# Kernel optimization log

Measured on AMD Instinct MI355X. Metric: run time of the kernel, lower is better.

## Reference

```python
import jax, jax.numpy as jnp
import numpy as np


def setup_inputs() -> dict:
    key = jax.random.key(0)
    k1, k2, k3 = jax.random.split(key, 3)
    T, B, C, H, W = 8, 4, 128, 96, 96
    h = w = 384  # original visibility-map resolution
    values = jax.random.normal(k1, (T + 1, B, C, H, W), jnp.float32)
    tvmap = jax.random.uniform(k2, (B, 1, h, w), jnp.float32)
    rvmaps = jax.random.uniform(k3, (T, B, 1, h, w), jnp.float32)
    return {"values": values, "tvmap": tvmap, "rvmaps": rvmaps}


def _resize_bin(m, H, W):
    # bilinear resize (half-pixel centers == torch align_corners=False), then > 0.5 threshold
    r = jax.image.resize(m, m.shape[:-2] + (H, W), method="bilinear")
    return (r > 0.5).astype(m.dtype)


def reference(values, tvmap, rvmaps):
    t_feat = values[0]          # [B,C,H,W]
    r_feats = values[1:]        # [T,B,C,H,W]
    T, B, C, H, W = r_feats.shape

    tv = _resize_bin(tvmap, H, W)                           # [B,1,H,W]
    rv = jax.vmap(lambda m: _resize_bin(m, H, W))(rvmaps)   # [T,B,1,H,W]
    vmap_ = tv[None] * rv                                   # [T,B,1,H,W]

    # per-frame masked similarity score gs
    gs = jnp.sum(vmap_ * t_feat[None] * r_feats, axis=(-1, -2, -3))  # [T,B]
    v_sum = jnp.sum(vmap_[:, :, 0], axis=(-1, -2))                   # [T,B]
    empty = v_sum < 1e-4
    gs = jnp.where(empty, 0.0, gs) / (v_sum + empty.astype(gs.dtype)) / C

    gss = gs.transpose(1, 0)[:, None, :, None, None]   # [B,1,T,1,1]
    vmaps = rv.transpose(1, 2, 0, 3, 4)                # [B,1,T,H,W]

    # masked softmax over frame axis (dim=2) with zero-guard
    mv = gss * vmaps
    mx = jnp.max(mv, axis=2, keepdims=True)
    me = jnp.exp(mv - mx) * vmaps
    ms = jnp.sum(me, axis=2, keepdims=True)
    ms = ms + (ms < 1e-4).astype(ms.dtype)
    c_match = jax.lax.stop_gradient(me / ms)           # [B,1,T,H,W]

    rf = r_feats.transpose(1, 2, 0, 3, 4)              # [B,C,T,H,W]
    c_out = jnp.sum(rf * c_match, axis=2)              # [B,C,H,W]

    c_mask = jnp.sum(c_match * vmaps, axis=2)          # [B,1,H,W]
    c_mask = jax.lax.stop_gradient(1.0 - jnp.mean(c_mask, axis=1, keepdims=True))

    out = jnp.concatenate([t_feat, c_out, c_mask], axis=1)  # [B, 2C+1, H, W]
    return out, c_mask, gs
```

## Files before the change

### kernel.cpp

```cpp
#include <hip/hip_runtime.h>
#include <math.h>

#define T_ 8
#define B_ 4
#define C_ 128
#define HW_ 9216
#define IN_HW_ 147456
#define NCHUNK 3

typedef float nfloat4 __attribute__((ext_vector_type(4)));

__device__ __forceinline__ double resize_px(const float* __restrict__ img, int y, int x) {
  static const double wm[8]  = {0.03125, 0.09375, 0.15625, 0.21875,
                                0.21875, 0.15625, 0.09375, 0.03125};
  static const double w0[8]  = {0.0, 0.0, 0.625/3.5, 0.875/3.5,
                                0.875/3.5, 0.625/3.5, 0.375/3.5, 0.125/3.5};
  static const double w95[8] = {0.125/3.5, 0.375/3.5, 0.625/3.5, 0.875/3.5,
                                0.875/3.5, 0.625/3.5, 0.0, 0.0};
  const double* wy = (y == 0) ? w0 : (y == 95 ? w95 : wm);
  const double* wx = (x == 0) ? w0 : (x == 95 ? w95 : wm);
  double acc = 0.0;
#pragma unroll
  for (int ky = 0; ky < 8; ++ky) {
    double wyv = wy[ky];
    if (wyv == 0.0) continue;
    int jy = 4 * y - 2 + ky;
    const float* row = img + jy * 384;
    double ra = 0.0;
#pragma unroll
    for (int kx = 0; kx < 8; ++kx) {
      double wxv = wx[kx];
      if (wxv == 0.0) continue;
      ra += wxv * (double)row[4 * x - 2 + kx];
    }
    acc += wyv * ra;
  }
  return acc;
}

__global__ __launch_bounds__(256) void k_masks(const float* __restrict__ tvmap,
                                               const float* __restrict__ rvmaps,
                                               float* __restrict__ rv,
                                               float* __restrict__ vm,
                                               float* __restrict__ v_part) {
  int tb = blockIdx.y;
  int b = tb % B_;
  int p = blockIdx.x * 256 + threadIdx.x;
  int y = p / 96, x = p % 96;
  float tvv = (resize_px(tvmap + (size_t)b * IN_HW_, y, x) > 0.5) ? 1.0f : 0.0f;
  float rvv = (resize_px(rvmaps + (size_t)tb * IN_HW_, y, x) > 0.5) ? 1.0f : 0.0f;
  float vmv = rvv * tvv;
  rv[(size_t)tb * HW_ + p] = rvv;
  vm[(size_t)tb * HW_ + p] = vmv;
  __shared__ float s[256];
  s[threadIdx.x] = vmv;
  __syncthreads();
  for (int k = 128; k > 0; k >>= 1) {
    if (threadIdx.x < (unsigned)k) s[threadIdx.x] += s[threadIdx.x + k];
    __syncthreads();
  }
  if (threadIdx.x == 0) v_part[tb * (HW_ / 256) + blockIdx.x] = s[0];
}

__global__ __launch_bounds__(256) void k_gs(const float* __restrict__ values,
                                            const float* __restrict__ vm,
                                            float* __restrict__ gs_part) {
  int c     = blockIdx.x;
  int chunk = blockIdx.y;
  int b     = blockIdx.z;
  const float4* tf = (const float4*)(values + ((size_t)b * C_ + c) * HW_);
  float acc[T_];
#pragma unroll
  for (int t = 0; t < T_; ++t) acc[t] = 0.f;
  int i0 = chunk * (HW_ / 4 / NCHUNK);
#pragma unroll 1
  for (int k = 0; k < HW_ / 4 / NCHUNK / 256; ++k) {
    int i = i0 + k * 256 + threadIdx.x;
    float4 a = tf[i];
#pragma unroll
    for (int t = 0; t < T_; ++t) {
      int tb = t * B_ + b;
      float4 m = ((const float4*)(vm + (size_t)tb * HW_))[i];
      float4 r = ((const float4*)(values + ((size_t)(B_ + tb) * C_ + c) * HW_))[i];
      acc[t] += m.x * a.x * r.x + m.y * a.y * r.y + m.z * a.z * r.z + m.w * a.w * r.w;
    }
  }
  __shared__ float part[4][T_];
  int lane = threadIdx.x & 63, wid = threadIdx.x >> 6;
#pragma unroll
  for (int t = 0; t < T_; ++t) {
    float v = acc[t];
    for (int off = 32; off > 0; off >>= 1) v += __shfl_down(v, off);
    if (lane == 0) part[wid][t] = v;
  }
  __syncthreads();
  if (threadIdx.x < T_) {
    int t = threadIdx.x;
    float v = part[0][t] + part[1][t] + part[2][t] + part[3][t];
    gs_part[(size_t)chunk * (T_ * B_ * C_) + (size_t)(t * B_ + b) * C_ + c] = v;
  }
}

__global__ void k_gsfin(const float* __restrict__ gs_part, const float* __restrict__ v_part,
                        float* __restrict__ gs, float* __restrict__ out_gs) {
  int i = threadIdx.x;
  if (i < T_ * B_) {
    float s = 0.f;
    for (int ch = 0; ch < NCHUNK; ++ch)
      for (int c = 0; c < C_; ++c)
        s += gs_part[(size_t)ch * (T_ * B_ * C_) + i * C_ + c];
    float vs = 0.f;
    for (int k = 0; k < HW_ / 256; ++k) vs += v_part[i * (HW_ / 256) + k];
    bool empty = vs < 1e-4f;
    float g = (empty ? 0.f : s) / (vs + (empty ? 1.f : 0.f)) / (float)C_;
    gs[i] = g;
    out_gs[i] = g;
  }
}

__global__ __launch_bounds__(256) void k_epi(const float* __restrict__ values,
                                             const float* __restrict__ rv,
                                             const float* __restrict__ gs,
                                             float* __restrict__ out,
                                             float* __restrict__ out_cmask) {
  int ctile = blockIdx.x;
  int ptile = blockIdx.y;
  int b     = blockIdx.z;
  __shared__ float gsh[T_];
  if (threadIdx.x < T_) gsh[threadIdx.x] = gs[threadIdx.x * B_ + b];
  __syncthreads();

  int p0 = ptile * 1024 + threadIdx.x * 4;

  float4 rv4[T_];
#pragma unroll
  for (int t = 0; t < T_; ++t)
    rv4[t] = *(const float4*)(rv + ((size_t)(t * B_ + b)) * HW_ + p0);

  float cm[T_][4];
  float cmask[4];
#pragma unroll
  for (int j = 0; j < 4; ++j) {
    float mv[T_];
    float mx = -1e30f;
#pragma unroll
    for (int t = 0; t < T_; ++t) {
      float rvv = ((const float*)&rv4[t])[j];
      mv[t] = gsh[t] * rvv;
      mx = fmaxf(mx, mv[t]);
    }
    float e[T_];
    float ms = 0.f;
#pragma unroll
    for (int t = 0; t < T_; ++t) {
      float rvv = ((const float*)&rv4[t])[j];
      e[t] = expf(mv[t] - mx) * rvv;
      ms += e[t];
    }
    if (ms < 1e-4f) ms += 1.f;
    float inv = 1.f / ms;
    float cs = 0.f;
#pragma unroll
    for (int t = 0; t < T_; ++t) {
      cm[t][j] = e[t] * inv;
      cs += cm[t][j] * ((const float*)&rv4[t])[j];
    }
    cmask[j] = 1.f - cs;
  }

  size_t outb = (size_t)b * 257 * HW_;
#pragma unroll 1
  for (int cc = 0; cc < 4; ++cc) {
    int c = ctile * 4 + cc;
    float4 tf = *(const float4*)(values + ((size_t)b * C_ + c) * HW_ + p0);
    nfloat4 tfn = {tf.x, tf.y, tf.z, tf.w};
    __builtin_nontemporal_store(tfn, (nfloat4*)(out + outb + (size_t)c * HW_ + p0));
    nfloat4 acc = {0.f, 0.f, 0.f, 0.f};
#pragma unroll
    for (int t = 0; t < T_; ++t) {
      const float4 r = *(const float4*)(values +
          ((size_t)((1 + t) * B_ + b) * C_ + c) * HW_ + p0);
      acc.x += cm[t][0] * r.x;
      acc.y += cm[t][1] * r.y;
      acc.z += cm[t][2] * r.z;
      acc.w += cm[t][3] * r.w;
    }
    __builtin_nontemporal_store(acc, (nfloat4*)(out + outb + (size_t)(C_ + c) * HW_ + p0));
  }
  if (ctile == 0) {
    nfloat4 cmv = {cmask[0], cmask[1], cmask[2], cmask[3]};
    __builtin_nontemporal_store(cmv, (nfloat4*)(out + outb + (size_t)256 * HW_ + p0));
    __builtin_nontemporal_store(cmv, (nfloat4*)(out_cmask + (size_t)b * HW_ + p0));
  }
}

extern "C" void kernel_launch(void* const* d_in, const int* in_sizes, int n_in,
                              void* d_out, int out_size, void* d_ws, size_t ws_size,
                              hipStream_t stream) {
  const float* values = (const float*)d_in[0];
  const float* tvmap  = (const float*)d_in[1];
  const float* rvmaps = (const float*)d_in[2];
  float* out = (float*)d_out;

  float* ws      = (float*)d_ws;
  float* rv      = ws;
  float* vm      = rv + (size_t)T_ * B_ * HW_;
  float* gs_part = vm + (size_t)T_ * B_ * HW_;
  float* v_part  = gs_part + NCHUNK * T_ * B_ * C_;
  float* gsar    = v_part + T_ * B_ * (HW_ / 256);

  float* out_cmask = out + (size_t)B_ * 257 * HW_;
  float* out_gs    = out_cmask + (size_t)B_ * HW_;

  hipLaunchKernelGGL(k_masks, dim3(HW_ / 256, T_ * B_), dim3(256), 0, stream,
                     tvmap, rvmaps, rv, vm, v_part);
  hipLaunchKernelGGL(k_gs,    dim3(C_, NCHUNK, B_),     dim3(256), 0, stream,
                     values, vm, gs_part);
  hipLaunchKernelGGL(k_gsfin, dim3(1),                  dim3(64),  0, stream,
                     gs_part, v_part, gsar, out_gs);
  hipLaunchKernelGGL(k_epi,   dim3(32, 9, B_),          dim3(256), 0, stream,
                     values, rv, gsar, out, out_cmask);
}
```

Measured before the change: 358.7 us.

## Fold gs finalization into epilogue kernel and split gs reduction into more chunks

Removes the single-block k_gsfin kernel. Each epilogue block now reduces the per-chunk gs partials and the visibility sums itself, using one 32-lane group per frame, and block (0,0) writes the gs output. The gs kernel goes from 3 chunks to 9, so each thread handles one float4 and the grid is larger. Nontemporal stores are replaced with plain stores. In exchange, the partial reduction is repeated redundantly in every epilogue block, and the switch to regular stores may change cache behaviour on the large output writes.

```diff
diff --git a/kernel.cpp b/kernel.cpp
--- a/kernel.cpp
+++ b/kernel.cpp
@@ -6,9 +6,8 @@
 #define C_ 128
 #define HW_ 9216
 #define IN_HW_ 147456
-#define NCHUNK 3
-
-typedef float nfloat4 __attribute__((ext_vector_type(4)));
+#define NCHUNK 9
+#define VPART 36
 
 __device__ __forceinline__ double resize_px(const float* __restrict__ img, int y, int x) {
   static const double wm[8]  = {0.03125, 0.09375, 0.15625, 0.21875,
@@ -59,7 +58,7 @@
     if (threadIdx.x < (unsigned)k) s[threadIdx.x] += s[threadIdx.x + k];
     __syncthreads();
   }
-  if (threadIdx.x == 0) v_part[tb * (HW_ / 256) + blockIdx.x] = s[0];
+  if (threadIdx.x == 0) v_part[tb * VPART + blockIdx.x] = s[0];
 }
 
 __global__ __launch_bounds__(256) void k_gs(const float* __restrict__ values,
@@ -68,22 +67,15 @@
   int c     = blockIdx.x;
   int chunk = blockIdx.y;
   int b     = blockIdx.z;
-  const float4* tf = (const float4*)(values + ((size_t)b * C_ + c) * HW_);
+  int i = chunk * (HW_ / 4 / NCHUNK) + threadIdx.x;
+  float4 a = ((const float4*)(values + ((size_t)b * C_ + c) * HW_))[i];
   float acc[T_];
 #pragma unroll
-  for (int t = 0; t < T_; ++t) acc[t] = 0.f;
-  int i0 = chunk * (HW_ / 4 / NCHUNK);
-#pragma unroll 1
-  for (int k = 0; k < HW_ / 4 / NCHUNK / 256; ++k) {
-    int i = i0 + k * 256 + threadIdx.x;
-    float4 a = tf[i];
-#pragma unroll
-    for (int t = 0; t < T_; ++t) {
-      int tb = t * B_ + b;
-      float4 m = ((const float4*)(vm + (size_t)tb * HW_))[i];
-      float4 r = ((const float4*)(values + ((size_t)(B_ + tb) * C_ + c) * HW_))[i];
-      acc[t] += m.x * a.x * r.x + m.y * a.y * r.y + m.z * a.z * r.z + m.w * a.w * r.w;
-    }
+  for (int t = 0; t < T_; ++t) {
+    int tb = t * B_ + b;
+    float4 m = ((const float4*)(vm + (size_t)tb * HW_))[i];
+    float4 r = ((const float4*)(values + ((size_t)(B_ + tb) * C_ + c) * HW_))[i];
+    acc[t] = m.x * a.x * r.x + m.y * a.y * r.y + m.z * a.z * r.z + m.w * a.w * r.w;
   }
   __shared__ float part[4][T_];
   int lane = threadIdx.x & 63, wid = threadIdx.x >> 6;
@@ -97,37 +89,44 @@
   if (threadIdx.x < T_) {
     int t = threadIdx.x;
     float v = part[0][t] + part[1][t] + part[2][t] + part[3][t];
-    gs_part[(size_t)chunk * (T_ * B_ * C_) + (size_t)(t * B_ + b) * C_ + c] = v;
-  }
-}
-
-__global__ void k_gsfin(const float* __restrict__ gs_part, const float* __restrict__ v_part,
-                        float* __restrict__ gs, float* __restrict__ out_gs) {
-  int i = threadIdx.x;
-  if (i < T_ * B_) {
-    float s = 0.f;
-    for (int ch = 0; ch < NCHUNK; ++ch)
-      for (int c = 0; c < C_; ++c)
-        s += gs_part[(size_t)ch * (T_ * B_ * C_) + i * C_ + c];
-    float vs = 0.f;
-    for (int k = 0; k < HW_ / 256; ++k) vs += v_part[i * (HW_ / 256) + k];
-    bool empty = vs < 1e-4f;
-    float g = (empty ? 0.f : s) / (vs + (empty ? 1.f : 0.f)) / (float)C_;
-    gs[i] = g;
-    out_gs[i] = g;
+    gs_part[((size_t)chunk * (T_ * B_) + (size_t)(t * B_ + b)) * C_ + c] = v;
   }
 }
 
 __global__ __launch_bounds__(256) void k_epi(const float* __restrict__ values,
                                              const float* __restrict__ rv,
-                                             const float* __restrict__ gs,
+                                             const float* __restrict__ gs_part,
+                                             const float* __restrict__ v_part,
                                              float* __restrict__ out,
-                                             float* __restrict__ out_cmask) {
+                                             float* __restrict__ out_cmask,
+                                             float* __restrict__ out_gs) {
   int ctile = blockIdx.x;
   int ptile = blockIdx.y;
   int b     = blockIdx.z;
+
   __shared__ float gsh[T_];
-  if (threadIdx.x < T_) gsh[threadIdx.x] = gs[threadIdx.x * B_ + b];
+  {
+    int t = threadIdx.x >> 5;
+    int lane = threadIdx.x & 31;
+    int tb = t * B_ + b;
+    float s = 0.f;
+    for (int idx = lane; idx < NCHUNK * C_; idx += 32) {
+      int ch = idx / C_, c = idx % C_;
+      s += gs_part[((size_t)ch * (T_ * B_) + tb) * C_ + c];
+    }
+    float vs = 0.f;
+    for (int k = lane; k < VPART; k += 32) vs += v_part[tb * VPART + k];
+    for (int off = 16; off > 0; off >>= 1) {
+      s  += __shfl_down(s, off, 32);
+      vs += __shfl_down(vs, off, 32);
+    }
+    if (lane == 0) {
+      bool empty = vs < 1e-4f;
+      float g = (empty ? 0.f : s) / (vs + (empty ? 1.f : 0.f)) / (float)C_;
+      gsh[t] = g;
+      if (ctile == 0 && ptile == 0) out_gs[t * B_ + b] = g;
+    }
+  }
   __syncthreads();
 
   int p0 = ptile * 1024 + threadIdx.x * 4;
@@ -173,9 +172,8 @@
   for (int cc = 0; cc < 4; ++cc) {
     int c = ctile * 4 + cc;
     float4 tf = *(const float4*)(values + ((size_t)b * C_ + c) * HW_ + p0);
-    nfloat4 tfn = {tf.x, tf.y, tf.z, tf.w};
-    __builtin_nontemporal_store(tfn, (nfloat4*)(out + outb + (size_t)c * HW_ + p0));
-    nfloat4 acc = {0.f, 0.f, 0.f, 0.f};
+    *(float4*)(out + outb + (size_t)c * HW_ + p0) = tf;
+    float4 acc = {0.f, 0.f, 0.f, 0.f};
 #pragma unroll
     for (int t = 0; t < T_; ++t) {
       const float4 r = *(const float4*)(values +
@@ -185,12 +183,12 @@
       acc.z += cm[t][2] * r.z;
       acc.w += cm[t][3] * r.w;
     }
-    __builtin_nontemporal_store(acc, (nfloat4*)(out + outb + (size_t)(C_ + c) * HW_ + p0));
+    *(float4*)(out + outb + (size_t)(C_ + c) * HW_ + p0) = acc;
   }
   if (ctile == 0) {
-    nfloat4 cmv = {cmask[0], cmask[1], cmask[2], cmask[3]};
-    __builtin_nontemporal_store(cmv, (nfloat4*)(out + outb + (size_t)256 * HW_ + p0));
-    __builtin_nontemporal_store(cmv, (nfloat4*)(out_cmask + (size_t)b * HW_ + p0));
+    float4 cmv = {cmask[0], cmask[1], cmask[2], cmask[3]};
+    *(float4*)(out + outb + (size_t)256 * HW_ + p0) = cmv;
+    *(float4*)(out_cmask + (size_t)b * HW_ + p0) = cmv;
   }
 }
 
@@ -206,8 +204,7 @@
   float* rv      = ws;
   float* vm      = rv + (size_t)T_ * B_ * HW_;
   float* gs_part = vm + (size_t)T_ * B_ * HW_;
-  float* v_part  = gs_part + NCHUNK * T_ * B_ * C_;
-  float* gsar    = v_part + T_ * B_ * (HW_ / 256);
+  float* v_part  = gs_part + (size_t)NCHUNK * T_ * B_ * C_;
 
   float* out_cmask = out + (size_t)B_ * 257 * HW_;
   float* out_gs    = out_cmask + (size_t)B_ * HW_;
@@ -216,8 +213,6 @@
                      tvmap, rvmaps, rv, vm, v_part);
   hipLaunchKernelGGL(k_gs,    dim3(C_, NCHUNK, B_),     dim3(256), 0, stream,
                      values, vm, gs_part);
-  hipLaunchKernelGGL(k_gsfin, dim3(1),                  dim3(64),  0, stream,
-                     gs_part, v_part, gsar, out_gs);
   hipLaunchKernelGGL(k_epi,   dim3(32, 9, B_),          dim3(256), 0, stream,
-                     values, rv, gsar, out, out_cmask);
-}
+                     values, rv, gs_part, v_part, out, out_cmask, out_gs);
+}
```

Measured after the change: 366.2 us. +2.1%, slower.
